# Kernel optimization log

Hardware: AMD Instinct MI355X
Metric: run time of the kernel (lower is better)

Reference implementation:

```python
import jax, jax.numpy as jnp
import numpy as np

KERNEL_NUM = 21
SIGMA = 0.1
EXACT_SIGMA = 0.001

def _kernel_params():
    mus, sigmas = [], []
    for i in range(KERNEL_NUM):
        mu = 1.0 / (KERNEL_NUM - 1) + 2.0 * i / (KERNEL_NUM - 1) - 1.0
        sigma = SIGMA
        if mu > 1.0:
            sigma = EXACT_SIGMA
            mu = 1.0
        mus.append(mu)
        sigmas.append(sigma)
    return np.asarray(mus, np.float32), np.asarray(sigmas, np.float32)

MU, SIG = _kernel_params()  # [K], [K]

def setup_inputs() -> dict:
    key = jax.random.key(0)
    k = jax.random.split(key, 8)
    V, D, B, L, R = 50000, 128, 512, 30, 200
    emb = jax.random.normal(k[0], (V, D), dtype=jnp.float32)
    W = jax.random.normal(k[1], (1, KERNEL_NUM), dtype=jnp.float32) * 0.1
    b = jax.random.normal(k[2], (1,), dtype=jnp.float32) * 0.1
    query1 = jax.random.randint(k[3], (B, L), 0, V, dtype=jnp.int32)
    doc1 = jax.random.randint(k[4], (B, R), 0, V, dtype=jnp.int32)
    query2 = jax.random.randint(k[5], (B, L), 0, V, dtype=jnp.int32)
    doc2 = jax.random.randint(k[6], (B, R), 0, V, dtype=jnp.int32)
    return {"emb": emb, "W": W, "b": b, "query1": query1, "doc1": doc1,
            "query2": query2, "doc2": doc2}

def _l2norm(x):
    # F.normalize(p=2, dim=-1): x / max(||x||, eps)
    n = jnp.sqrt(jnp.sum(x * x, axis=-1, keepdims=True))
    return x / jnp.maximum(n, 1e-12)

def _predict(emb, W, b, q, d):
    eq = _l2norm(emb[q])              # [B,L,D]
    ed = _l2norm(emb[d])              # [B,R,D]
    M = jnp.einsum('bld,brd->blr', eq, ed)  # matching matrix [B,L,R]
    # multi-Gaussian kernel bank: [B,L,R,K]
    Kmat = jnp.exp(-0.5 * (M[..., None] - MU) ** 2 / (SIG ** 2))
    km = jnp.sum(jnp.log1p(jnp.sum(Kmat, axis=2)), axis=1)  # [B,K]
    return km @ W.T + b               # [B,1]

def reference(emb, W, b, query1, doc1, query2, doc2):
    logits1 = _predict(emb, W, b, query1, doc1)
    logits2 = _predict(emb, W, b, query2, doc2)
    return jax.nn.sigmoid(logits1 - logits2)
```

## Files before the change

kernel.cpp:

```cpp
#include <hip/hip_runtime.h>
#include <math.h>

#define V   50000
#define DIM 128
#define BB  512
#define LQ  30
#define RD  200
#define KN  21

typedef unsigned short ushort_t;
typedef __attribute__((ext_vector_type(8))) short bf16x8;
typedef __attribute__((ext_vector_type(4))) float f32x4;
typedef __attribute__((ext_vector_type(2))) float f32x2;

#if __has_builtin(__builtin_amdgcn_exp2f)
#define EXP2F(x) __builtin_amdgcn_exp2f(x)
#else
#define EXP2F(x) __expf((x) * 0.69314718f)
#endif

#define ALPHA 72.1347520f
#define E10   22026.4657948f

static __device__ __forceinline__ ushort_t f2bf(float x) {
    unsigned u = __builtin_bit_cast(unsigned, x);
    return (ushort_t)((u + 0x7FFFu + ((u >> 16) & 1u)) >> 16);
}
static __device__ __forceinline__ bf16x8 as_frag(int4 v) {
    return __builtin_bit_cast(bf16x8, v);
}

__global__ __launch_bounds__(256) void knrm_norm(const float* __restrict__ emb,
                                                 ushort_t* __restrict__ nh) {
    int row = blockIdx.x * 8 + (threadIdx.x >> 5);
    int c4  = (threadIdx.x & 31) * 4;
    const float4 v = *reinterpret_cast<const float4*>(emb + (size_t)row * DIM + c4);
    float ss = v.x * v.x + v.y * v.y + v.z * v.z + v.w * v.w;
#pragma unroll
    for (int off = 1; off < 32; off <<= 1) ss += __shfl_xor(ss, off);
    float inv = 1.0f / fmaxf(sqrtf(ss), 1e-12f);
    uint2 o;
    o.x = (unsigned)f2bf(v.x * inv) | ((unsigned)f2bf(v.y * inv) << 16);
    o.y = (unsigned)f2bf(v.z * inv) | ((unsigned)f2bf(v.w * inv) << 16);
    *reinterpret_cast<uint2*>(nh + (size_t)row * DIM + c4) = o;
}

static __device__ __forceinline__ void bank4_pk(float4 pv, int4 dt, int qt,
                                                f32x2* ks2, float& cnt) {
    const float mv[4] = {pv.x, pv.y, pv.z, pv.w};
    const int   dv[4] = {dt.x, dt.y, dt.z, dt.w};
    f32x2 t[4], u[4];
#pragma unroll
    for (int i = 0; i < 4; ++i) {
        float m  = mv[i];
        float dA = m + 0.5f, dB = m - 0.5f;
        float tA = EXP2F(-ALPHA * dA * (dA + 0.9f));
        float tB = EXP2F(-ALPHA * dB * (dB + 0.9f));
        float uB = EXP2F(14.4269504f * dB);
        float uA = uB * E10;
        t[i] = f32x2{tA, tB};
        u[i] = f32x2{uA, uB};
        cnt += (dv[i] == qt) ? 1.0f : 0.0f;
    }
#pragma unroll
    for (int k = 0; k < 10; ++k) {
        ks2[k] += (t[0] + t[1]) + (t[2] + t[3]);
        t[0] *= u[0]; t[1] *= u[1]; t[2] *= u[2]; t[3] *= u[3];
    }
}

static __device__ __forceinline__ void load_frag4(const ushort_t* base, int4* f) {
    f[0] = *reinterpret_cast<const int4*>(base);
    f[1] = *reinterpret_cast<const int4*>(base + 32);
    f[2] = *reinterpret_cast<const int4*>(base + 64);
    f[3] = *reinterpret_cast<const int4*>(base + 96);
}

__global__ __launch_bounds__(256) void knrm_main(
    const ushort_t* __restrict__ nh,
    const int* __restrict__ q1, const int* __restrict__ d1,
    const int* __restrict__ q2, const int* __restrict__ d2,
    float* __restrict__ partial)
{
    __shared__ __align__(16) char smem[10752];
    float (*P)[68] = reinterpret_cast<float (*)[68]>(smem);
    float* kredw   = reinterpret_cast<float*>(smem);
    __shared__ int sQtok[32];
    __shared__ int sDtok[128];

    const int pb = blockIdx.x, y = blockIdx.y;
    const int pair = pb >> 9, b = pb & 511;
    const int* qind = (pair ? q2 : q1) + b * LQ;
    const int* dind = (pair ? d2 : d1) + b * RD;
    const int cb = y * 128;

    const int tid = threadIdx.x;
    const int lane = tid & 63, wave = tid >> 6;
    const int r = lane & 15, g = lane >> 4;
    const int rt = wave & 1, half = wave >> 1;

    if (tid < 32)  sQtok[tid] = (tid < LQ) ? qind[tid] : -2;
    if (tid < 128) { int c = cb + tid; sDtok[tid] = (c < RD) ? dind[c] : -1; }

    const int qrow = rt * 16 + r;
    const int qi = qind[qrow < LQ ? qrow : LQ - 1];
    int4 qh[4];
    load_frag4(nh + (size_t)qi * DIM + g * 8, qh);

    const int c64_0 = cb, c64_1 = cb + 64;
    const int dr0a = c64_0 + half * 32 + r,  dr0b = dr0a + 16;
    const int dr1a = c64_1 + half * 32 + r,  dr1b = dr1a + 16;
    const int di0a = dind[dr0a < RD ? dr0a : RD - 1];
    const int di0b = dind[dr0b < RD ? dr0b : RD - 1];

    f32x2 ks2[10];
#pragma unroll
    for (int k = 0; k < 10; ++k) ks2[k] = f32x2{0.f, 0.f};
    float cnt = 0.0f;

    const int brow = tid & 31;
    const int c0   = (tid >> 5) * 4;
    const int prow0 = rt * 16 + g * 4;

    {
        int4 d0[4], d1[4];
        load_frag4(nh + (size_t)di0a * DIM + g * 8, d0);
        load_frag4(nh + (size_t)di0b * DIM + g * 8, d1);
        f32x4 acc0 = {0.f, 0.f, 0.f, 0.f}, acc1 = {0.f, 0.f, 0.f, 0.f};
#pragma unroll
        for (int ks = 0; ks < 4; ++ks) {
            bf16x8 ah = as_frag(qh[ks]);
            acc0 = __builtin_amdgcn_mfma_f32_16x16x32_bf16(ah, as_frag(d0[ks]), acc0, 0, 0, 0);
            acc1 = __builtin_amdgcn_mfma_f32_16x16x32_bf16(ah, as_frag(d1[ks]), acc1, 0, 0, 0);
        }
#pragma unroll
        for (int j = 0; j < 4; ++j) {
            P[prow0 + j][half * 32 + r]      = acc0[j];
            P[prow0 + j][half * 32 + 16 + r] = acc1[j];
        }
    }
    __syncthreads();

    int4 e0[4], e1[4];
    {
        const int di1a = dind[dr1a < RD ? dr1a : RD - 1];
        const int di1b = dind[dr1b < RD ? dr1b : RD - 1];
        load_frag4(nh + (size_t)di1a * DIM + g * 8, e0);
        load_frag4(nh + (size_t)di1b * DIM + g * 8, e1);
    }

    if (brow < LQ && c64_0 + c0 < RD) {
        const int qt = sQtok[brow];
        float4 p0 = *reinterpret_cast<const float4*>(&P[brow][c0]);
        int4  dt0 = *reinterpret_cast<const int4*>(&sDtok[c0]);
        bank4_pk(p0, dt0, qt, ks2, cnt);
        if (c64_0 + c0 + 32 < RD) {
            float4 p1 = *reinterpret_cast<const float4*>(&P[brow][c0 + 32]);
            int4  dt1 = *reinterpret_cast<const int4*>(&sDtok[c0 + 32]);
            bank4_pk(p1, dt1, qt, ks2, cnt);
        }
    }

    f32x4 acc0 = {0.f, 0.f, 0.f, 0.f}, acc1 = {0.f, 0.f, 0.f, 0.f};
#pragma unroll
    for (int ks = 0; ks < 4; ++ks) {
        bf16x8 ah = as_frag(qh[ks]);
        acc0 = __builtin_amdgcn_mfma_f32_16x16x32_bf16(ah, as_frag(e0[ks]), acc0, 0, 0, 0);
        acc1 = __builtin_amdgcn_mfma_f32_16x16x32_bf16(ah, as_frag(e1[ks]), acc1, 0, 0, 0);
    }
    __syncthreads();
#pragma unroll
    for (int j = 0; j < 4; ++j) {
        P[prow0 + j][half * 32 + r]      = acc0[j];
        P[prow0 + j][half * 32 + 16 + r] = acc1[j];
    }
    __syncthreads();

    if (brow < LQ && c64_1 + c0 < RD) {
        const int qt = sQtok[brow];
        float4 p0 = *reinterpret_cast<const float4*>(&P[brow][c0]);
        int4  dt0 = *reinterpret_cast<const int4*>(&sDtok[64 + c0]);
        bank4_pk(p0, dt0, qt, ks2, cnt);
        if (c64_1 + c0 + 32 < RD) {
            float4 p1 = *reinterpret_cast<const float4*>(&P[brow][c0 + 32]);
            int4  dt1 = *reinterpret_cast<const int4*>(&sDtok[64 + c0 + 32]);
            bank4_pk(p1, dt1, qt, ks2, cnt);
        }
    }
    __syncthreads();

#pragma unroll
    for (int k = 0; k < 10; ++k) {
        float va = ks2[k].x + __shfl_xor(ks2[k].x, 32);
        float vb = ks2[k].y + __shfl_xor(ks2[k].y, 32);
        ks2[k] = f32x2{va, vb};
    }
    cnt += __shfl_xor(cnt, 32);
    if (lane < 32) {
        const int base = (wave * 32 + lane) * KN;
#pragma unroll
        for (int k = 0; k < 10; ++k) {
            kredw[base + k]      = ks2[k].x;
            kredw[base + 10 + k] = ks2[k].y;
        }
        kredw[base + 20] = cnt;
    }
    __syncthreads();

    float* dst = partial + ((size_t)pb * 2 + y) * (LQ * KN);
    for (int e = tid; e < LQ * KN; e += 256) {
        int row = e / KN, k = e - row * KN;
        float s = kredw[row * KN + k] + kredw[(32 + row) * KN + k]
                + kredw[(64 + row) * KN + k] + kredw[(96 + row) * KN + k];
        float sc = 1.0f;
        if (k < 20) {
            float j = (float)((k < 10) ? k : k - 10) - 4.5f;
            sc = EXP2F(-0.721347520f * j * j);
        }
        dst[e] = sc * s;
    }
}

__global__ __launch_bounds__(128) void knrm_finish(const float* __restrict__ partial,
                                                   const float* __restrict__ W,
                                                   float* __restrict__ out) {
    __shared__ float red[2];
    const int b = blockIdx.x, tid = threadIdx.x;
    float s = 0.0f;
    for (int e = tid; e < LQ * KN; e += 128) {
        int row = e / KN, k = e - row * KN;
        float s1 = partial[((size_t)b * 2 + 0) * (LQ * KN) + e]
                 + partial[((size_t)b * 2 + 1) * (LQ * KN) + e];
        float s2 = partial[((size_t)(BB + b) * 2 + 0) * (LQ * KN) + e]
                 + partial[((size_t)(BB + b) * 2 + 1) * (LQ * KN) + e];
        s += W[k] * (log1pf(s1) - log1pf(s2));
    }
#pragma unroll
    for (int off = 1; off < 64; off <<= 1) s += __shfl_xor(s, off);
    if ((tid & 63) == 0) red[tid >> 6] = s;
    __syncthreads();
    if (tid == 0) {
        float logit = red[0] + red[1];
        out[b] = 1.0f / (1.0f + expf(-logit));
    }
}

extern "C" void kernel_launch(void* const* d_in, const int* in_sizes, int n_in,
                              void* d_out, int out_size, void* d_ws, size_t ws_size,
                              hipStream_t stream) {
    const float* emb = (const float*)d_in[0];
    const float* W   = (const float*)d_in[1];
    const int* q1    = (const int*)d_in[3];
    const int* dd1   = (const int*)d_in[4];
    const int* q2    = (const int*)d_in[5];
    const int* dd2   = (const int*)d_in[6];

    float* partial = (float*)d_ws;
    ushort_t* nh   = (ushort_t*)(partial + 2048 * LQ * KN);

    knrm_norm<<<V / 8, 256, 0, stream>>>(emb, nh);
    dim3 grid(1024, 2);
    knrm_main<<<grid, 256, 0, stream>>>(nh, q1, dd1, q2, dd2, partial);
    knrm_finish<<<BB, 128, 0, stream>>>(partial, W, (float*)d_out);
}
```

Before: 41.38 us.

## Split doc columns into four 64-wide blocks instead of two pipelined 128-wide blocks

```diff
diff --git a/kernel.cpp b/kernel.cpp
--- a/kernel.cpp
+++ b/kernel.cpp
@@ -86,89 +86,41 @@
     float (*P)[68] = reinterpret_cast<float (*)[68]>(smem);
     float* kredw   = reinterpret_cast<float*>(smem);
     __shared__ int sQtok[32];
-    __shared__ int sDtok[128];
+    __shared__ __align__(16) int sDtok[64];
 
     const int pb = blockIdx.x, y = blockIdx.y;
     const int pair = pb >> 9, b = pb & 511;
     const int* qind = (pair ? q2 : q1) + b * LQ;
     const int* dind = (pair ? d2 : d1) + b * RD;
-    const int cb = y * 128;
+    const int cb = y * 64;
 
     const int tid = threadIdx.x;
     const int lane = tid & 63, wave = tid >> 6;
     const int r = lane & 15, g = lane >> 4;
     const int rt = wave & 1, half = wave >> 1;
 
-    if (tid < 32)  sQtok[tid] = (tid < LQ) ? qind[tid] : -2;
-    if (tid < 128) { int c = cb + tid; sDtok[tid] = (c < RD) ? dind[c] : -1; }
+    if (tid < 32) sQtok[tid] = (tid < LQ) ? qind[tid] : -2;
+    if (tid < 64) { int c = cb + tid; sDtok[tid] = (c < RD) ? dind[c] : -1; }
 
     const int qrow = rt * 16 + r;
     const int qi = qind[qrow < LQ ? qrow : LQ - 1];
-    int4 qh[4];
+    const int dra = cb + half * 32 + r, drb = dra + 16;
+    const int dia = dind[dra < RD ? dra : RD - 1];
+    const int dib = dind[drb < RD ? drb : RD - 1];
+
+    int4 qh[4], dfa[4], dfb[4];
     load_frag4(nh + (size_t)qi * DIM + g * 8, qh);
-
-    const int c64_0 = cb, c64_1 = cb + 64;
-    const int dr0a = c64_0 + half * 32 + r,  dr0b = dr0a + 16;
-    const int dr1a = c64_1 + half * 32 + r,  dr1b = dr1a + 16;
-    const int di0a = dind[dr0a < RD ? dr0a : RD - 1];
-    const int di0b = dind[dr0b < RD ? dr0b : RD - 1];
-
-    f32x2 ks2[10];
-#pragma unroll
-    for (int k = 0; k < 10; ++k) ks2[k] = f32x2{0.f, 0.f};
-    float cnt = 0.0f;
-
-    const int brow = tid & 31;
-    const int c0   = (tid >> 5) * 4;
-    const int prow0 = rt * 16 + g * 4;
-
-    {
-        int4 d0[4], d1[4];
-        load_frag4(nh + (size_t)di0a * DIM + g * 8, d0);
-        load_frag4(nh + (size_t)di0b * DIM + g * 8, d1);
-        f32x4 acc0 = {0.f, 0.f, 0.f, 0.f}, acc1 = {0.f, 0.f, 0.f, 0.f};
-#pragma unroll
-        for (int ks = 0; ks < 4; ++ks) {
-            bf16x8 ah = as_frag(qh[ks]);
-            acc0 = __builtin_amdgcn_mfma_f32_16x16x32_bf16(ah, as_frag(d0[ks]), acc0, 0, 0, 0);
-            acc1 = __builtin_amdgcn_mfma_f32_16x16x32_bf16(ah, as_frag(d1[ks]), acc1, 0, 0, 0);
-        }
-#pragma unroll
-        for (int j = 0; j < 4; ++j) {
-            P[prow0 + j][half * 32 + r]      = acc0[j];
-            P[prow0 + j][half * 32 + 16 + r] = acc1[j];
-        }
-    }
-    __syncthreads();
-
-    int4 e0[4], e1[4];
-    {
-        const int di1a = dind[dr1a < RD ? dr1a : RD - 1];
-        const int di1b = dind[dr1b < RD ? dr1b : RD - 1];
-        load_frag4(nh + (size_t)di1a * DIM + g * 8, e0);
-        load_frag4(nh + (size_t)di1b * DIM + g * 8, e1);
-    }
-
-    if (brow < LQ && c64_0 + c0 < RD) {
-        const int qt = sQtok[brow];
-        float4 p0 = *reinterpret_cast<const float4*>(&P[brow][c0]);
-        int4  dt0 = *reinterpret_cast<const int4*>(&sDtok[c0]);
-        bank4_pk(p0, dt0, qt, ks2, cnt);
-        if (c64_0 + c0 + 32 < RD) {
-            float4 p1 = *reinterpret_cast<const float4*>(&P[brow][c0 + 32]);
-            int4  dt1 = *reinterpret_cast<const int4*>(&sDtok[c0 + 32]);
-            bank4_pk(p1, dt1, qt, ks2, cnt);
-        }
-    }
+    load_frag4(nh + (size_t)dia * DIM + g * 8, dfa);
+    load_frag4(nh + (size_t)dib * DIM + g * 8, dfb);
 
     f32x4 acc0 = {0.f, 0.f, 0.f, 0.f}, acc1 = {0.f, 0.f, 0.f, 0.f};
 #pragma unroll
     for (int ks = 0; ks < 4; ++ks) {
         bf16x8 ah = as_frag(qh[ks]);
-        acc0 = __builtin_amdgcn_mfma_f32_16x16x32_bf16(ah, as_frag(e0[ks]), acc0, 0, 0, 0);
-        acc1 = __builtin_amdgcn_mfma_f32_16x16x32_bf16(ah, as_frag(e1[ks]), acc1, 0, 0, 0);
-    }
-    __syncthreads();
+        acc0 = __builtin_amdgcn_mfma_f32_16x16x32_bf16(ah, as_frag(dfa[ks]), acc0, 0, 0, 0);
+        acc1 = __builtin_amdgcn_mfma_f32_16x16x32_bf16(ah, as_frag(dfb[ks]), acc1, 0, 0, 0);
+    }
+    const int prow0 = rt * 16 + g * 4;
 #pragma unroll
     for (int j = 0; j < 4; ++j) {
         P[prow0 + j][half * 32 + r]      = acc0[j];
@@ -176,15 +128,21 @@
     }
     __syncthreads();
 
-    if (brow < LQ && c64_1 + c0 < RD) {
+    const int brow = tid & 31;
+    const int c0   = (tid >> 5) * 4;
+    f32x2 ks2[10];
+#pragma unroll
+    for (int k = 0; k < 10; ++k) ks2[k] = f32x2{0.f, 0.f};
+    float cnt = 0.0f;
+
+    const int4* sDtok4 = (const int4*)sDtok;
+    if (brow < LQ && cb + c0 < RD) {
         const int qt = sQtok[brow];
         float4 p0 = *reinterpret_cast<const float4*>(&P[brow][c0]);
-        int4  dt0 = *reinterpret_cast<const int4*>(&sDtok[64 + c0]);
-        bank4_pk(p0, dt0, qt, ks2, cnt);
-        if (c64_1 + c0 + 32 < RD) {
+        bank4_pk(p0, sDtok4[c0 >> 2], qt, ks2, cnt);
+        if (cb + c0 + 32 < RD) {
             float4 p1 = *reinterpret_cast<const float4*>(&P[brow][c0 + 32]);
-            int4  dt1 = *reinterpret_cast<const int4*>(&sDtok[64 + c0 + 32]);
-            bank4_pk(p1, dt1, qt, ks2, cnt);
+            bank4_pk(p1, sDtok4[(c0 + 32) >> 2], qt, ks2, cnt);
         }
     }
     __syncthreads();
@@ -207,7 +165,7 @@
     }
     __syncthreads();
 
-    float* dst = partial + ((size_t)pb * 2 + y) * (LQ * KN);
+    float* dst = partial + ((size_t)pb * 4 + y) * (LQ * KN);
     for (int e = tid; e < LQ * KN; e += 256) {
         int row = e / KN, k = e - row * KN;
         float s = kredw[row * KN + k] + kredw[(32 + row) * KN + k]
@@ -226,13 +184,13 @@
                                                    float* __restrict__ out) {
     __shared__ float red[2];
     const int b = blockIdx.x, tid = threadIdx.x;
+    const float* p1 = partial + (size_t)b * 4 * (LQ * KN);
+    const float* p2 = partial + (size_t)(BB + b) * 4 * (LQ * KN);
     float s = 0.0f;
     for (int e = tid; e < LQ * KN; e += 128) {
         int row = e / KN, k = e - row * KN;
-        float s1 = partial[((size_t)b * 2 + 0) * (LQ * KN) + e]
-                 + partial[((size_t)b * 2 + 1) * (LQ * KN) + e];
-        float s2 = partial[((size_t)(BB + b) * 2 + 0) * (LQ * KN) + e]
-                 + partial[((size_t)(BB + b) * 2 + 1) * (LQ * KN) + e];
+        float s1 = p1[e] + p1[LQ * KN + e] + p1[2 * LQ * KN + e] + p1[3 * LQ * KN + e];
+        float s2 = p2[e] + p2[LQ * KN + e] + p2[2 * LQ * KN + e] + p2[3 * LQ * KN + e];
         s += W[k] * (log1pf(s1) - log1pf(s2));
     }
 #pragma unroll
@@ -256,10 +214,10 @@
     const int* dd2   = (const int*)d_in[6];
 
     float* partial = (float*)d_ws;
-    ushort_t* nh   = (ushort_t*)(partial + 2048 * LQ * KN);
+    ushort_t* nh   = (ushort_t*)(partial + (size_t)1024 * 4 * LQ * KN);
 
     knrm_norm<<<V / 8, 256, 0, stream>>>(emb, nh);
-    dim3 grid(1024, 2);
+    dim3 grid(1024, 4);
     knrm_main<<<grid, 256, 0, stream>>>(nh, q1, dd1, q2, dd2, partial);
     knrm_finish<<<BB, 128, 0, stream>>>(partial, W, (float*)d_out);
 }
```

New measurement: 43.41 us. +4.9%, slower.
